# Kernel tuning notes

Hardware: AMD Instinct MI355X
Metric: run time of the kernel (lower is better)

The kernel has to match this reference:

```python
import jax, jax.numpy as jnp
import numpy as np

N_HEADS = 16
D_QKV = 128
THETA = 10000.0


def setup_inputs() -> dict:
    key = jax.random.key(0)
    k1, k2, k3 = jax.random.split(key, 3)
    B, L, d_model = 2, 2048, 2048
    X = jax.random.normal(k1, (B, L, d_model), jnp.float32)
    # torch Linear weight is (out,in); we store the transposed (in,out) layout so y = X @ W
    W_qkv = jax.random.normal(k2, (d_model, 3 * N_HEADS * D_QKV), jnp.float32) / np.sqrt(d_model)
    W_out = jax.random.normal(k3, (N_HEADS * D_QKV, d_model), jnp.float32) / np.sqrt(N_HEADS * D_QKV)
    return {"X": X, "W_qkv": W_qkv, "W_out": W_out}


def _rope(x, cos, sin):
    # interleaved-pair RoPE (rotary-embedding-torch style): pairs are (x[2i], x[2i+1])
    x1 = x[..., 0::2]
    x2 = x[..., 1::2]
    out = jnp.stack([x1 * cos - x2 * sin, x1 * sin + x2 * cos], axis=-1)
    return out.reshape(x.shape)


def reference(X, W_qkv, W_out):
    B, L, _ = X.shape
    H, D = N_HEADS, D_QKV
    # fused QKV projection; layout per head is [q|k|v] of size 3*D (matches 'b l (h ddd)')
    qkv = (X @ W_qkv).reshape(B, L, H, 3 * D).transpose(0, 2, 1, 3)  # b h l 3d
    Q, K, V = jnp.split(qkv, 3, axis=-1)                              # each b h l d
    inv_freq = 1.0 / (THETA ** (jnp.arange(0, D, 2, dtype=jnp.float32) / D))
    ang = jnp.arange(L, dtype=jnp.float32)[:, None] * inv_freq[None, :]  # (L, D/2)
    cos, sin = jnp.cos(ang), jnp.sin(ang)
    Q = _rope(Q, cos, sin)
    K = _rope(K, cos, sin)
    # causal SDPA
    scores = jnp.einsum('bhqd,bhkd->bhqk', Q, K) / jnp.sqrt(jnp.float32(D))
    causal = jnp.tril(jnp.ones((L, L), dtype=bool))
    scores = jnp.where(causal, scores, -jnp.inf)
    attn = jax.nn.softmax(scores, axis=-1)
    out = jnp.einsum('bhqk,bhkd->bqhd', attn, V).reshape(B, L, H * D)
    return out @ W_out
```

## Files before the change

kernel.cpp:

```cpp
#include <hip/hip_runtime.h>

typedef __bf16 bf16x8 __attribute__((ext_vector_type(8)));
typedef float f32x4 __attribute__((ext_vector_type(4)));

#define LSEQ 2048

__device__ __forceinline__ unsigned short f2b(float f){
  unsigned u = __builtin_bit_cast(unsigned, f);
  u += 0x7FFFu + ((u >> 16) & 1u);
  return (unsigned short)(u >> 16);
}
__device__ __forceinline__ float b2f(unsigned short h){
  unsigned u = ((unsigned)h) << 16;
  return __builtin_bit_cast(float, u);
}

typedef __attribute__((address_space(1))) const unsigned int glb_u32;
typedef __attribute__((address_space(3))) unsigned int lds_u32;
__device__ __forceinline__ void gld_lds16(const void* g, void* l){
  __builtin_amdgcn_global_load_lds((glb_u32*)g, (lds_u32*)l, 16, 0, 0);
}

__global__ __launch_bounds__(256) void cvt_f32_bf16(const float* __restrict__ in,
                                                    unsigned short* __restrict__ out){
  int tid = blockIdx.x * 256 + threadIdx.x;
  float4 v = reinterpret_cast<const float4*>(in)[tid];
  ushort4 o;
  o.x = f2b(v.x); o.y = f2b(v.y); o.z = f2b(v.z); o.w = f2b(v.w);
  reinterpret_cast<ushort4*>(out)[tid] = o;
}

__global__ __launch_bounds__(256) void transpose_cvt(const float* __restrict__ in,
                                                     unsigned short* __restrict__ out,
                                                     int R, int C){
  __shared__ float t[32][33];
  int c0 = blockIdx.x * 32, r0 = blockIdx.y * 32;
  int tx = threadIdx.x, ty = threadIdx.y;
  #pragma unroll
  for (int i = 0; i < 4; i++){
    int r = ty + i*8;
    t[r][tx] = in[(size_t)(r0 + r) * C + c0 + tx];
  }
  __syncthreads();
  #pragma unroll
  for (int i = 0; i < 4; i++){
    int c = ty + i*8;
    out[(size_t)(c0 + c) * R + r0 + tx] = f2b(t[tx][c]);
  }
}

__global__ __launch_bounds__(256) void trig_init(float* __restrict__ cosT,
                                                 float* __restrict__ sinT){
  int tid = blockIdx.x * 256 + threadIdx.x;
  int i = tid & 63; int l = tid >> 6;
  float invf = powf(10000.0f, -((float)(2*i)) / 128.0f);
  float ang = (float)l * invf;
  cosT[tid] = cosf(ang);
  sinT[tid] = sinf(ang);
}

__global__ __launch_bounds__(256) void rope_qk(const unsigned short* __restrict__ qkv,
                                               const float* __restrict__ cosT,
                                               const float* __restrict__ sinT,
                                               unsigned short* __restrict__ Qr,
                                               unsigned short* __restrict__ Kr){
  int tid = blockIdx.x * 256 + threadIdx.x;
  int i  = tid & 63;
  int l  = (tid >> 6) & (LSEQ - 1);
  int bh = tid >> 17;
  int b = bh >> 4, h = bh & 15;
  size_t base = (size_t)(b*LSEQ + l) * 6144 + h*384;
  float c = cosT[l*64 + i], s = sinT[l*64 + i];
  float q1 = b2f(qkv[base + 2*i]),       q2 = b2f(qkv[base + 2*i + 1]);
  float k1 = b2f(qkv[base + 128 + 2*i]), k2 = b2f(qkv[base + 128 + 2*i + 1]);
  const float qs = 0.12751691f;
  size_t ob = ((size_t)bh*LSEQ + l) * 128;
  Qr[ob + 2*i]     = f2b((q1*c - q2*s) * qs);
  Qr[ob + 2*i + 1] = f2b((q1*s + q2*c) * qs);
  Kr[ob + 2*i]     = f2b(k1*c - k2*s);
  Kr[ob + 2*i + 1] = f2b(k1*s + k2*c);
}

__global__ __launch_bounds__(256) void vtrans(const unsigned short* __restrict__ qkv,
                                              unsigned short* __restrict__ Vt){
  __shared__ unsigned short t[64][65];
  int d0 = blockIdx.x * 64, l0 = blockIdx.y * 64, bh = blockIdx.z;
  int b = bh >> 4, h = bh & 15;
  int tx = threadIdx.x, ty = threadIdx.y;
  #pragma unroll
  for (int i = 0; i < 16; i++){
    int lr = ty + i*4;
    t[lr][tx] = qkv[(size_t)(b*LSEQ + l0 + lr) * 6144 + h*384 + 256 + d0 + tx];
  }
  __syncthreads();
  #pragma unroll
  for (int i = 0; i < 16; i++){
    int dr = ty + i*4;
    Vt[(size_t)(bh*128 + d0 + dr) * LSEQ + l0 + tx] = t[tx][dr];
  }
}

template<bool BF16_OUT>
__global__ __launch_bounds__(256) void gemm_bt(const unsigned short* __restrict__ A,
                                               const unsigned short* __restrict__ Bt,
                                               void* __restrict__ Cp,
                                               int M, int N, int K){
  __shared__ __align__(16) unsigned short As[128*64];
  __shared__ __align__(16) unsigned short Bs[128*64];
  int m0 = blockIdx.y * 128, n0 = blockIdx.x * 128;
  int tid = threadIdx.x, lane = tid & 63, wave = tid >> 6;
  int wm = wave >> 1, wn = wave & 1;
  int lr = lane & 15, lh = lane >> 4;
  int r8 = lane >> 3;
  int cg = (lane & 7) ^ r8;
  f32x4 acc[4][4];
  #pragma unroll
  for (int a = 0; a < 4; a++)
    #pragma unroll
    for (int bb = 0; bb < 4; bb++)
      acc[a][bb] = (f32x4){0.f, 0.f, 0.f, 0.f};

  const unsigned short* Abase = A  + (size_t)(m0 + wave*32 + r8)*K + cg*8;
  const unsigned short* Bbase = Bt + (size_t)(n0 + wave*32 + r8)*K + cg*8;

  int nk = K >> 6;
  for (int k0 = 0; k0 < nk; k0++){
    __syncthreads();
    #pragma unroll
    for (int i = 0; i < 4; i++){
      gld_lds16(Abase + (size_t)i*8*K + k0*64, &As[(wave*32 + i*8)*64]);
      gld_lds16(Bbase + (size_t)i*8*K + k0*64, &Bs[(wave*32 + i*8)*64]);
    }
    __syncthreads();
    #pragma unroll
    for (int kk = 0; kk < 2; kk++){
      bf16x8 af[4], bfg[4];
      #pragma unroll
      for (int f = 0; f < 4; f++){
        int ra = wm*64 + f*16 + lr;
        af[f]  = *reinterpret_cast<const bf16x8*>(&As[ra*64 + (((kk*4 + lh) ^ (ra & 7)) * 8)]);
        int rb = wn*64 + f*16 + lr;
        bfg[f] = *reinterpret_cast<const bf16x8*>(&Bs[rb*64 + (((kk*4 + lh) ^ (rb & 7)) * 8)]);
      }
      __builtin_amdgcn_s_setprio(1);
      #pragma unroll
      for (int fm = 0; fm < 4; fm++)
        #pragma unroll
        for (int fn = 0; fn < 4; fn++)
          acc[fm][fn] = __builtin_amdgcn_mfma_f32_16x16x32_bf16(af[fm], bfg[fn], acc[fm][fn], 0, 0, 0);
      __builtin_amdgcn_s_setprio(0);
    }
  }
  #pragma unroll
  for (int fm = 0; fm < 4; fm++)
    #pragma unroll
    for (int fn = 0; fn < 4; fn++)
      #pragma unroll
      for (int r = 0; r < 4; r++){
        int row = m0 + wm*64 + fm*16 + lh*4 + r;
        int col = n0 + wn*64 + fn*16 + lr;
        float v = acc[fm][fn][r];
        if (BF16_OUT) ((unsigned short*)Cp)[(size_t)row*N + col] = f2b(v);
        else          ((float*)Cp)[(size_t)row*N + col] = v;
      }
}

__global__ __launch_bounds__(256) void attn_kernel(const unsigned short* __restrict__ Qr,
                                                   const unsigned short* __restrict__ Kr,
                                                   const unsigned short* __restrict__ Vt,
                                                   unsigned short* __restrict__ aout){
  __shared__ __align__(16) unsigned short Ks[2][64*128];
  __shared__ __align__(16) unsigned short Vs[2][128*64];
  __shared__ __align__(16) unsigned short Ps[4][2][16*64];
  int bh = blockIdx.x;
  int q0 = (15 - (int)blockIdx.y) * 128;
  int tid = threadIdx.x;
  int wave = tid >> 6, lane = tid & 63;
  int lr = lane & 15, lh = lane >> 4;
  int b = bh >> 4, h = bh & 15;

  bf16x8 qf[2][4];
  #pragma unroll
  for (int g = 0; g < 2; g++){
    const unsigned short* Qb = Qr + ((size_t)bh*LSEQ + q0 + wave*32 + g*16 + lr) * 128;
    #pragma unroll
    for (int kc = 0; kc < 4; kc++)
      qf[g][kc] = *reinterpret_cast<const bf16x8*>(Qb + kc*32 + lh*8);
  }

  float m_i[2][4], l_i[2][4];
  f32x4 o[2][8];
  #pragma unroll
  for (int g = 0; g < 2; g++)
    #pragma unroll
    for (int r = 0; r < 4; r++){ m_i[g][r] = -__builtin_inff(); l_i[g][r] = 0.f; }
  #pragma unroll
  for (int g = 0; g < 2; g++)
    #pragma unroll
    for (int nd = 0; nd < 8; nd++) o[g][nd] = (f32x4){0.f, 0.f, 0.f, 0.f};

  const unsigned short* Kbh = Kr + (size_t)bh*LSEQ*128;
  const unsigned short* Vbh = Vt + (size_t)bh*128*LSEQ;
  int klrow = lane >> 4;
  int vlrow = lane >> 3;
  int vg = (lane & 7) ^ vlrow;

  int ntiles = (q0 >> 6) + 2;

  {
    #pragma unroll
    for (int i = 0; i < 4; i++){
      int rk = wave*16 + i*4 + klrow;
      int gk = (lane & 15) ^ (rk & 7);
      gld_lds16(Kbh + (size_t)rk*128 + gk*8, &Ks[0][(wave*16 + i*4)*128]);
      int rv = wave*32 + i*8 + vlrow;
      gld_lds16(Vbh + (size_t)rv*LSEQ + vg*8, &Vs[0][(wave*32 + i*8)*64]);
    }
  }
  __syncthreads();

  int cur = 0;
  for (int t = 0; t < ntiles; t++){
    if (t + 1 < ntiles){
      int kv1 = (t + 1) * 64;
      #pragma unroll
      for (int i = 0; i < 4; i++){
        int rk = wave*16 + i*4 + klrow;
        int gk = (lane & 15) ^ (rk & 7);
        gld_lds16(Kbh + (size_t)(kv1 + rk)*128 + gk*8, &Ks[cur^1][(wave*16 + i*4)*128]);
        int rv = wave*32 + i*8 + vlrow;
        gld_lds16(Vbh + (size_t)rv*LSEQ + kv1 + vg*8, &Vs[cur^1][(wave*32 + i*8)*64]);
      }
    }
    int kv0 = t * 64;

    f32x4 s[2][4];
    #pragma unroll
    for (int g = 0; g < 2; g++)
      #pragma unroll
      for (int nc = 0; nc < 4; nc++)
        s[g][nc] = (f32x4){0.f, 0.f, 0.f, 0.f};
    __builtin_amdgcn_s_setprio(1);
    #pragma unroll
    for (int nc = 0; nc < 4; nc++){
      int n = nc*16 + lr;
      #pragma unroll
      for (int kc = 0; kc < 4; kc++){
        bf16x8 kf = *reinterpret_cast<const bf16x8*>(&Ks[cur][n*128 + (((kc*4 + lh) ^ (n & 7)) * 8)]);
        s[0][nc] = __builtin_amdgcn_mfma_f32_16x16x32_bf16(qf[0][kc], kf, s[0][nc], 0, 0, 0);
        s[1][nc] = __builtin_amdgcn_mfma_f32_16x16x32_bf16(qf[1][kc], kf, s[1][nc], 0, 0, 0);
      }
    }
    __builtin_amdgcn_s_setprio(0);

    if (t >= ntiles - 2){
      #pragma unroll
      for (int g = 0; g < 2; g++)
        #pragma unroll
        for (int nc = 0; nc < 4; nc++)
          #pragma unroll
          for (int r = 0; r < 4; r++){
            int q  = q0 + wave*32 + g*16 + lh*4 + r;
            int kv = kv0 + nc*16 + lr;
            if (kv > q) s[g][nc][r] = -__builtin_inff();
          }
    }

    #pragma unroll
    for (int g = 0; g < 2; g++){
      float pm[4];
      #pragma unroll
      for (int r = 0; r < 4; r++)
        pm[r] = fmaxf(fmaxf(s[g][0][r], s[g][1][r]), fmaxf(s[g][2][r], s[g][3][r]));
      #pragma unroll
      for (int off = 1; off < 16; off <<= 1)
        #pragma unroll
        for (int r = 0; r < 4; r++)
          pm[r] = fmaxf(pm[r], __shfl_xor(pm[r], off, 64));
      float al[4], rs[4];
      #pragma unroll
      for (int r = 0; r < 4; r++){
        float mn = fmaxf(m_i[g][r], pm[r]);
        al[r] = exp2f(m_i[g][r] - mn);
        m_i[g][r] = mn;
        rs[r] = 0.f;
      }
      #pragma unroll
      for (int nc = 0; nc < 4; nc++)
        #pragma unroll
        for (int r = 0; r < 4; r++){
          float p = exp2f(s[g][nc][r] - m_i[g][r]);
          s[g][nc][r] = p;
          rs[r] += p;
        }
      #pragma unroll
      for (int off = 1; off < 16; off <<= 1)
        #pragma unroll
        for (int r = 0; r < 4; r++)
          rs[r] += __shfl_xor(rs[r], off, 64);
      #pragma unroll
      for (int r = 0; r < 4; r++)
        l_i[g][r] = l_i[g][r]*al[r] + rs[r];
      #pragma unroll
      for (int nd = 0; nd < 8; nd++)
        #pragma unroll
        for (int r = 0; r < 4; r++)
          o[g][nd][r] *= al[r];
      #pragma unroll
      for (int nc = 0; nc < 4; nc++)
        #pragma unroll
        for (int r = 0; r < 4; r++){
          int m = lh*4 + r;
          int col = nc*16 + lr;
          Ps[wave][g][m*64 + (((col >> 3) ^ (m & 7)) * 8) + (col & 7)] = f2b(s[g][nc][r]);
        }
    }

    __builtin_amdgcn_s_setprio(1);
    #pragma unroll
    for (int kc = 0; kc < 2; kc++){
      bf16x8 pa0 = *reinterpret_cast<const bf16x8*>(&Ps[wave][0][lr*64 + (((kc*4 + lh) ^ (lr & 7)) * 8)]);
      bf16x8 pa1 = *reinterpret_cast<const bf16x8*>(&Ps[wave][1][lr*64 + (((kc*4 + lh) ^ (lr & 7)) * 8)]);
      #pragma unroll
      for (int nd = 0; nd < 8; nd++){
        int d = nd*16 + lr;
        bf16x8 vf = *reinterpret_cast<const bf16x8*>(&Vs[cur][d*64 + (((kc*4 + lh) ^ (d & 7)) * 8)]);
        o[0][nd] = __builtin_amdgcn_mfma_f32_16x16x32_bf16(pa0, vf, o[0][nd], 0, 0, 0);
        o[1][nd] = __builtin_amdgcn_mfma_f32_16x16x32_bf16(pa1, vf, o[1][nd], 0, 0, 0);
      }
    }
    __builtin_amdgcn_s_setprio(0);

    __syncthreads();
    cur ^= 1;
  }

  #pragma unroll
  for (int g = 0; g < 2; g++){
    float inv[4];
    #pragma unroll
    for (int r = 0; r < 4; r++) inv[r] = 1.0f / l_i[g][r];
    #pragma unroll
    for (int nd = 0; nd < 8; nd++)
      #pragma unroll
      for (int r = 0; r < 4; r++){
        int q = q0 + wave*32 + g*16 + lh*4 + r;
        aout[((size_t)b*LSEQ + q)*2048 + h*128 + nd*16 + lr] = f2b(o[g][nd][r] * inv[r]);
      }
  }
}

extern "C" void kernel_launch(void* const* d_in, const int* in_sizes, int n_in,
                              void* d_out, int out_size, void* d_ws, size_t ws_size,
                              hipStream_t stream){
  const float* X  = (const float*)d_in[0];
  const float* Wq = (const float*)d_in[1];
  const float* Wo = (const float*)d_in[2];
  float* out = (float*)d_out;
  char* ws = (char*)d_ws;
  unsigned short* Xb   = (unsigned short*)(ws + 0);
  unsigned short* Wt   = (unsigned short*)(ws + 16777216);
  unsigned short* Wot  = (unsigned short*)(ws + 41943040);
  unsigned short* QKV  = (unsigned short*)(ws + 50331648);
  unsigned short* Kr   = (unsigned short*)(ws + 100663296);
  unsigned short* Vt   = (unsigned short*)(ws + 117440512);
  float* cosT          = (float*)(ws + 134217728);
  float* sinT          = (float*)(ws + 134742016);
  unsigned short* Qr   = Xb;
  unsigned short* Aout = QKV;

  cvt_f32_bf16<<<8192, 256, 0, stream>>>(X, Xb);
  transpose_cvt<<<dim3(192, 64), dim3(32, 8), 0, stream>>>(Wq, Wt, 2048, 6144);
  transpose_cvt<<<dim3(64, 64),  dim3(32, 8), 0, stream>>>(Wo, Wot, 2048, 2048);
  trig_init<<<512, 256, 0, stream>>>(cosT, sinT);
  gemm_bt<true><<<dim3(48, 32), 256, 0, stream>>>(Xb, Wt, (void*)QKV, 4096, 6144, 2048);
  rope_qk<<<16384, 256, 0, stream>>>(QKV, cosT, sinT, Qr, Kr);
  vtrans<<<dim3(2, 32, 32), dim3(64, 4), 0, stream>>>(QKV, Vt);
  attn_kernel<<<dim3(32, 16), 256, 0, stream>>>(Qr, Kr, Vt, Aout);
  gemm_bt<false><<<dim3(16, 32), 256, 0, stream>>>(Aout, Wot, (void*)out, 4096, 2048, 2048);
}
```

Baseline: 421.7 us.

## Transpose QK^T MFMA so softmax rows are lane-local, pack P with cvt_pk

Swaps the operands of the QK^T MFMA so each lane holds scores for a single query row. The row max and sum then need only two cross-lane shuffles instead of four per register, and probabilities are packed into bf16 pairs with v_cvt_pk_bf16_f32 and written to LDS as 32-bit words. The rescale factors are shuffled back to match the PV accumulator layout. The q-block ordering across blockIdx.y is also changed to interleave long and short causal blocks for better load balance.

```diff
diff --git a/kernel.cpp b/kernel.cpp
--- a/kernel.cpp
+++ b/kernel.cpp
@@ -13,6 +13,11 @@
 __device__ __forceinline__ float b2f(unsigned short h){
   unsigned u = ((unsigned)h) << 16;
   return __builtin_bit_cast(float, u);
+}
+__device__ __forceinline__ unsigned cvt_pk_bf16(float lo, float hi){
+  unsigned r;
+  asm("v_cvt_pk_bf16_f32 %0, %1, %2" : "=v"(r) : "v"(lo), "v"(hi));
+  return r;
 }
 
 typedef __attribute__((address_space(1))) const unsigned int glb_u32;
@@ -173,7 +178,9 @@
   __shared__ __align__(16) unsigned short Vs[2][128*64];
   __shared__ __align__(16) unsigned short Ps[4][2][16*64];
   int bh = blockIdx.x;
-  int q0 = (15 - (int)blockIdx.y) * 128;
+  int y = blockIdx.y;
+  int qi = (y < 8) ? (15 - y) : (y - 8);
+  int q0 = qi * 128;
   int tid = threadIdx.x;
   int wave = tid >> 6, lane = tid & 63;
   int lr = lane & 15, lh = lane >> 4;
@@ -188,12 +195,10 @@
       qf[g][kc] = *reinterpret_cast<const bf16x8*>(Qb + kc*32 + lh*8);
   }
 
-  float m_i[2][4], l_i[2][4];
+  float m_i[2], l_i[2];
   f32x4 o[2][8];
   #pragma unroll
-  for (int g = 0; g < 2; g++)
-    #pragma unroll
-    for (int r = 0; r < 4; r++){ m_i[g][r] = -__builtin_inff(); l_i[g][r] = 0.f; }
+  for (int g = 0; g < 2; g++){ m_i[g] = -__builtin_inff(); l_i[g] = 0.f; }
   #pragma unroll
   for (int g = 0; g < 2; g++)
     #pragma unroll
@@ -204,18 +209,17 @@
   int klrow = lane >> 4;
   int vlrow = lane >> 3;
   int vg = (lane & 7) ^ vlrow;
+  int srcb = (lane & 48) + ((lane >> 2) & 12);
 
   int ntiles = (q0 >> 6) + 2;
 
-  {
-    #pragma unroll
-    for (int i = 0; i < 4; i++){
-      int rk = wave*16 + i*4 + klrow;
-      int gk = (lane & 15) ^ (rk & 7);
-      gld_lds16(Kbh + (size_t)rk*128 + gk*8, &Ks[0][(wave*16 + i*4)*128]);
-      int rv = wave*32 + i*8 + vlrow;
-      gld_lds16(Vbh + (size_t)rv*LSEQ + vg*8, &Vs[0][(wave*32 + i*8)*64]);
-    }
+  #pragma unroll
+  for (int i = 0; i < 4; i++){
+    int rk = wave*16 + i*4 + klrow;
+    int gk = (lane & 15) ^ (rk & 7);
+    gld_lds16(Kbh + (size_t)rk*128 + gk*8, &Ks[0][(wave*16 + i*4)*128]);
+    int rv = wave*32 + i*8 + vlrow;
+    gld_lds16(Vbh + (size_t)rv*LSEQ + vg*8, &Vs[0][(wave*32 + i*8)*64]);
   }
   __syncthreads();
 
@@ -247,8 +251,8 @@
       #pragma unroll
       for (int kc = 0; kc < 4; kc++){
         bf16x8 kf = *reinterpret_cast<const bf16x8*>(&Ks[cur][n*128 + (((kc*4 + lh) ^ (n & 7)) * 8)]);
-        s[0][nc] = __builtin_amdgcn_mfma_f32_16x16x32_bf16(qf[0][kc], kf, s[0][nc], 0, 0, 0);
-        s[1][nc] = __builtin_amdgcn_mfma_f32_16x16x32_bf16(qf[1][kc], kf, s[1][nc], 0, 0, 0);
+        s[0][nc] = __builtin_amdgcn_mfma_f32_16x16x32_bf16(kf, qf[0][kc], s[0][nc], 0, 0, 0);
+        s[1][nc] = __builtin_amdgcn_mfma_f32_16x16x32_bf16(kf, qf[1][kc], s[1][nc], 0, 0, 0);
       }
     }
     __builtin_amdgcn_s_setprio(0);
@@ -260,71 +264,63 @@
         for (int nc = 0; nc < 4; nc++)
           #pragma unroll
           for (int r = 0; r < 4; r++){
-            int q  = q0 + wave*32 + g*16 + lh*4 + r;
-            int kv = kv0 + nc*16 + lr;
+            int kv = kv0 + nc*16 + lh*4 + r;
+            int q  = q0 + wave*32 + g*16 + lr;
             if (kv > q) s[g][nc][r] = -__builtin_inff();
           }
     }
 
     #pragma unroll
     for (int g = 0; g < 2; g++){
-      float pm[4];
-      #pragma unroll
-      for (int r = 0; r < 4; r++)
-        pm[r] = fmaxf(fmaxf(s[g][0][r], s[g][1][r]), fmaxf(s[g][2][r], s[g][3][r]));
-      #pragma unroll
-      for (int off = 1; off < 16; off <<= 1)
-        #pragma unroll
-        for (int r = 0; r < 4; r++)
-          pm[r] = fmaxf(pm[r], __shfl_xor(pm[r], off, 64));
-      float al[4], rs[4];
-      #pragma unroll
-      for (int r = 0; r < 4; r++){
-        float mn = fmaxf(m_i[g][r], pm[r]);
-        al[r] = exp2f(m_i[g][r] - mn);
-        m_i[g][r] = mn;
-        rs[r] = 0.f;
-      }
+      float pm = -__builtin_inff();
       #pragma unroll
       for (int nc = 0; nc < 4; nc++)
-        #pragma unroll
-        for (int r = 0; r < 4; r++){
-          float p = exp2f(s[g][nc][r] - m_i[g][r]);
-          s[g][nc][r] = p;
-          rs[r] += p;
-        }
-      #pragma unroll
-      for (int off = 1; off < 16; off <<= 1)
-        #pragma unroll
-        for (int r = 0; r < 4; r++)
-          rs[r] += __shfl_xor(rs[r], off, 64);
-      #pragma unroll
-      for (int r = 0; r < 4; r++)
-        l_i[g][r] = l_i[g][r]*al[r] + rs[r];
+        pm = fmaxf(pm, fmaxf(fmaxf(s[g][nc][0], s[g][nc][1]), fmaxf(s[g][nc][2], s[g][nc][3])));
+      pm = fmaxf(pm, __shfl_xor(pm, 16, 64));
+      pm = fmaxf(pm, __shfl_xor(pm, 32, 64));
+      float mn = fmaxf(m_i[g], pm);
+      float al = exp2f(m_i[g] - mn);
+      m_i[g] = mn;
+      float rs = 0.f;
+      unsigned w[8];
+      #pragma unroll
+      for (int nc = 0; nc < 4; nc++){
+        float p0 = exp2f(s[g][nc][0] - mn), p1 = exp2f(s[g][nc][1] - mn);
+        float p2 = exp2f(s[g][nc][2] - mn), p3 = exp2f(s[g][nc][3] - mn);
+        rs += (p0 + p1) + (p2 + p3);
+        w[nc*2]     = cvt_pk_bf16(p0, p1);
+        w[nc*2 + 1] = cvt_pk_bf16(p2, p3);
+      }
+      rs += __shfl_xor(rs, 16, 64);
+      rs += __shfl_xor(rs, 32, 64);
+      l_i[g] = l_i[g]*al + rs;
+      float al_r[4];
+      #pragma unroll
+      for (int r = 0; r < 4; r++) al_r[r] = __shfl(al, srcb + r, 64);
       #pragma unroll
       for (int nd = 0; nd < 8; nd++)
         #pragma unroll
         for (int r = 0; r < 4; r++)
-          o[g][nd][r] *= al[r];
+          o[g][nd][r] *= al_r[r];
       #pragma unroll
       for (int nc = 0; nc < 4; nc++)
         #pragma unroll
-        for (int r = 0; r < 4; r++){
-          int m = lh*4 + r;
-          int col = nc*16 + lr;
-          Ps[wave][g][m*64 + (((col >> 3) ^ (m & 7)) * 8) + (col & 7)] = f2b(s[g][nc][r]);
+        for (int hh = 0; hh < 2; hh++){
+          int kvg = nc*2 + (lh >> 1);
+          int klo = (lh & 1)*4 + 2*hh;
+          *reinterpret_cast<unsigned*>(&Ps[wave][g][lr*64 + ((kvg ^ (lr & 7)) << 3) + klo]) = w[nc*2 + hh];
         }
     }
 
     __builtin_amdgcn_s_setprio(1);
     #pragma unroll
     for (int kc = 0; kc < 2; kc++){
-      bf16x8 pa0 = *reinterpret_cast<const bf16x8*>(&Ps[wave][0][lr*64 + (((kc*4 + lh) ^ (lr & 7)) * 8)]);
-      bf16x8 pa1 = *reinterpret_cast<const bf16x8*>(&Ps[wave][1][lr*64 + (((kc*4 + lh) ^ (lr & 7)) * 8)]);
+      bf16x8 pa0 = *reinterpret_cast<const bf16x8*>(&Ps[wave][0][lr*64 + (((kc*4 + lh) ^ (lr & 7)) << 3)]);
+      bf16x8 pa1 = *reinterpret_cast<const bf16x8*>(&Ps[wave][1][lr*64 + (((kc*4 + lh) ^ (lr & 7)) << 3)]);
       #pragma unroll
       for (int nd = 0; nd < 8; nd++){
         int d = nd*16 + lr;
-        bf16x8 vf = *reinterpret_cast<const bf16x8*>(&Vs[cur][d*64 + (((kc*4 + lh) ^ (d & 7)) * 8)]);
+        bf16x8 vf = *reinterpret_cast<const bf16x8*>(&Vs[cur][d*64 + (((kc*4 + lh) ^ (d & 7)) << 3)]);
         o[0][nd] = __builtin_amdgcn_mfma_f32_16x16x32_bf16(pa0, vf, o[0][nd], 0, 0, 0);
         o[1][nd] = __builtin_amdgcn_mfma_f32_16x16x32_bf16(pa1, vf, o[1][nd], 0, 0, 0);
       }
@@ -337,15 +333,16 @@
 
   #pragma unroll
   for (int g = 0; g < 2; g++){
-    float inv[4];
-    #pragma unroll
-    for (int r = 0; r < 4; r++) inv[r] = 1.0f / l_i[g][r];
+    float inv = 1.0f / l_i[g];
+    float inv_r[4];
+    #pragma unroll
+    for (int r = 0; r < 4; r++) inv_r[r] = __shfl(inv, srcb + r, 64);
     #pragma unroll
     for (int nd = 0; nd < 8; nd++)
       #pragma unroll
       for (int r = 0; r < 4; r++){
         int q = q0 + wave*32 + g*16 + lh*4 + r;
-        aout[((size_t)b*LSEQ + q)*2048 + h*128 + nd*16 + lr] = f2b(o[g][nd][r] * inv[r]);
+        aout[((size_t)b*LSEQ + q)*2048 + h*128 + nd*16 + lr] = f2b(o[g][nd][r] * inv_r[r]);
       }
   }
 }
```

Measured after the change: 420.6 us. No clear change (-0.3%).
